# Kernel tuning notes

Measured on AMD Instinct MI355X. Metric: run time of the kernel, lower is better.

The kernel has to match this reference:

```python
import jax, jax.numpy as jnp
import numpy as np

DT = 0.1


def setup_inputs() -> dict:
    key = jax.random.key(0)
    k1, k2, k3, k4 = jax.random.split(key, 4)
    B, T, I, H, O = 32, 1024, 256, 512, 256
    return {
        "x": jax.random.normal(k1, (B, T, I), dtype=jnp.float32),
        "input_weights": jax.random.normal(k2, (H, I), dtype=jnp.float32) * (1.0 / np.sqrt(I)),
        "recurrent_weights": jax.random.normal(k3, (H, H), dtype=jnp.float32) * (1.0 / np.sqrt(H)),
        "time_constants": jnp.ones((H,), dtype=jnp.float32) + 0.1,
        "output_weights": jax.random.normal(k4, (O, H), dtype=jnp.float32) * (1.0 / np.sqrt(H)),
        "bias": jnp.zeros((H,), dtype=jnp.float32),
    }


def reference(x, input_weights, recurrent_weights, time_constants, output_weights, bias):
    B = x.shape[0]
    H = recurrent_weights.shape[0]
    h0 = jnp.zeros((B, H), dtype=x.dtype)

    # Precompute the input projection for all timesteps at once: (B,T,I)@(I,H) -> (T,B,H)
    sensory_all = jnp.einsum("bti,hi->tbh", x, input_weights)

    def step(hidden, sensory):
        # sensory: (B, H)
        recurrent = hidden @ recurrent_weights.T                      # (B, H)
        adaptive_tau = jax.nn.softplus(
            time_constants + 0.1 * jnp.mean(jnp.abs(sensory), axis=0)
        )                                                             # (H,)
        activation = jnp.tanh(sensory + recurrent + bias)             # (B, H)
        dhidden_dt = -hidden / adaptive_tau[None, :] + activation
        hidden = hidden + DT * dhidden_dt
        out_t = hidden @ output_weights.T                             # (B, O)
        return hidden, out_t

    final_hidden, outputs = jax.lax.scan(step, h0, sensory_all)        # outputs: (T, B, O)
    output = jnp.transpose(outputs, (1, 0, 2))                          # (B, T, O)
    return output, final_hidden
```

## Files before the change

### kernel.cpp

```cpp
#include <hip/hip_runtime.h>
#include <cstddef>

#define B_ 32
#define T_ 1024
#define IN_ 256
#define H_ 512
#define O_ 256
#define DT_ 0.1f

typedef _Float16 half2_t __attribute__((ext_vector_type(2)));

__device__ __forceinline__ float fdot2(half2_t a, half2_t b, float c) {
#if defined(__has_builtin)
#if __has_builtin(__builtin_amdgcn_fdot2)
    return __builtin_amdgcn_fdot2(a, b, c, false);
#else
    return c + (float)a[0] * (float)b[0] + (float)a[1] * (float)b[1];
#endif
#else
    return c + (float)a[0] * (float)b[0] + (float)a[1] * (float)b[1];
#endif
}

__device__ __forceinline__ half2_t cvt2(float x, float y) {
    half2_t r; r[0] = (_Float16)x; r[1] = (_Float16)y; return r;
}

__device__ __forceinline__ half2_t as_h2(float f) {
    union { float f; half2_t h; } u; u.f = f; return u.h;
}

template<int N, int K, bool SWA, bool SWC>
__global__ __launch_bounds__(256, 4) void gemm128(const float* __restrict__ A,
                                                  const float* __restrict__ Bw,
                                                  float* __restrict__ C) {
    __shared__ float al[32][132];
    __shared__ float bl[32][132];
    const int tid = threadIdx.x;
    const int m0 = blockIdx.x * 128;
    const int n0 = blockIdx.y * 128;
    const int tx = tid & 15;
    const int ty = tid >> 4;
    float acc[8][8] = {};

    const int lrow = tid >> 3;
    const int kk = (tid & 7) * 4;

    for (int kc = 0; kc < K; kc += 32) {
        __syncthreads();
#pragma unroll
        for (int p = 0; p < 4; ++p) {
            const int row = lrow + p * 32;
            const int m = m0 + row;
            const size_t aoff = SWA ? ((size_t)((m & 31) * T_ + (m >> 5)) * K)
                                    : ((size_t)m * K);
            const float4 v = *(const float4*)(A + aoff + kc + kk);
            al[kk + 0][row] = v.x; al[kk + 1][row] = v.y;
            al[kk + 2][row] = v.z; al[kk + 3][row] = v.w;
        }
#pragma unroll
        for (int p = 0; p < 4; ++p) {
            const int row = lrow + p * 32;
            const float4 v = *(const float4*)(Bw + (size_t)(n0 + row) * K + kc + kk);
            bl[kk + 0][row] = v.x; bl[kk + 1][row] = v.y;
            bl[kk + 2][row] = v.z; bl[kk + 3][row] = v.w;
        }
        __syncthreads();
#pragma unroll
        for (int k = 0; k < 32; ++k) {
            float av[8], bv[8];
            *(float4*)&av[0] = *(const float4*)&al[k][ty * 8];
            *(float4*)&av[4] = *(const float4*)&al[k][ty * 8 + 4];
            *(float4*)&bv[0] = *(const float4*)&bl[k][tx * 8];
            *(float4*)&bv[4] = *(const float4*)&bl[k][tx * 8 + 4];
#pragma unroll
            for (int i = 0; i < 8; ++i)
#pragma unroll
                for (int j = 0; j < 8; ++j)
                    acc[i][j] = fmaf(av[i], bv[j], acc[i][j]);
        }
    }
#pragma unroll
    for (int i = 0; i < 8; ++i) {
        const int m = m0 + ty * 8 + i;
        const size_t coff = SWC ? ((size_t)((m & 31) * T_ + (m >> 5)) * N)
                                : ((size_t)m * N);
        const float4 v0 = make_float4(acc[i][0], acc[i][1], acc[i][2], acc[i][3]);
        const float4 v1 = make_float4(acc[i][4], acc[i][5], acc[i][6], acc[i][7]);
        *(float4*)(C + coff + n0 + tx * 8) = v0;
        *(float4*)(C + coff + n0 + tx * 8 + 4) = v1;
    }
}

__global__ __launch_bounds__(512) void tau_kernel(const float* __restrict__ sens,
                                                  const float* __restrict__ tc,
                                                  float* __restrict__ acoef) {
    const int t = blockIdx.x;
    const int h = threadIdx.x;
    float s = 0.f;
#pragma unroll 8
    for (int b = 0; b < B_; ++b)
        s += fabsf(sens[((size_t)t * B_ + b) * H_ + h]);
    const float x = tc[h] + 0.1f * (s * (1.f / 32.f));
    const float sp = fmaxf(x, 0.f) + log1pf(expf(-fabsf(x)));
    acoef[(size_t)t * H_ + h] = 1.f - DT_ / sp;
}

#define RG_ 12
#define LG_ 4
#define SMEM_W   131072
#define SMEM_P   8192
#define SMEM_H   1024
#define SMEM_TOT (SMEM_W + SMEM_P + SMEM_H)

__global__ __launch_bounds__(512, 2) void scan_kernel(
    const float* __restrict__ Wr, const float* __restrict__ acoef,
    const float* __restrict__ bias, float* sensH, float* __restrict__ finalh) {
    extern __shared__ char smem[];
    half2_t* wlds = (half2_t*)smem;
    float* pred   = (float*)(smem + SMEM_W);
    _Float16* h2s = (_Float16*)(smem + SMEM_W + SMEM_P);

    const int tid = threadIdx.x;
    const int b = blockIdx.x;
    const int w = tid >> 6;
    const int c = w >> 1;
    const int rg = ((w & 1) << 6) | (tid & 63);
    const int row0 = rg * 4;
    const int col0 = c * 128;

    half2_t wr[4][RG_ * 4];
#pragma unroll
    for (int r = 0; r < 4; ++r) {
        const float* wrow = Wr + (size_t)(row0 + r) * H_ + col0;
#pragma unroll
        for (int d = 0; d < RG_ * 4; ++d) {
            const float2 v = *(const float2*)(wrow + 2 * d);
            wr[r][d] = cvt2(v.x, v.y);
        }
#pragma unroll
        for (int g = 0; g < LG_; ++g) {
#pragma unroll
            for (int j = 0; j < 4; ++j) {
                const float2 v = *(const float2*)(wrow + 2 * ((RG_ + g) * 4 + j));
                wlds[((size_t)(g * 4 + r) * 512 + tid) * 4 + j] = cvt2(v.x, v.y);
            }
        }
    }

    if (tid < 256) ((half2_t*)h2s)[tid] = cvt2(0.f, 0.f);
    float h_reg = 0.f;
    const float bias_r = bias[tid];
    float s_cur = sensH[(size_t)b * H_ + tid];
    float a_cur = acoef[tid];
    __syncthreads();

    const half2_t* h2c = (const half2_t*)h2s + c * 64;

    for (int t = 0; t < T_; ++t) {
        const int tn = (t < T_ - 1) ? t + 1 : t;
        const float s_nxt = sensH[((size_t)tn * B_ + b) * H_ + tid];
        const float a_nxt = acoef[(size_t)tn * H_ + tid];

        float acc[4] = {0.f, 0.f, 0.f, 0.f};
#pragma unroll
        for (int g = 0; g < RG_; ++g) {
            const float4 hv = *(const float4*)(h2c + g * 4);
            const half2_t hh[4] = {as_h2(hv.x), as_h2(hv.y), as_h2(hv.z), as_h2(hv.w)};
#pragma unroll
            for (int r = 0; r < 4; ++r)
#pragma unroll
                for (int j = 0; j < 4; ++j)
                    acc[r] = fdot2(wr[r][g * 4 + j], hh[j], acc[r]);
        }
#pragma unroll
        for (int g = 0; g < LG_; ++g) {
            const float4 hv = *(const float4*)(h2c + (RG_ + g) * 4);
            const half2_t hh[4] = {as_h2(hv.x), as_h2(hv.y), as_h2(hv.z), as_h2(hv.w)};
#pragma unroll
            for (int r = 0; r < 4; ++r) {
                const float4 wv = *(const float4*)(wlds + ((size_t)(g * 4 + r) * 512 + tid) * 4);
                acc[r] = fdot2(as_h2(wv.x), hh[0], acc[r]);
                acc[r] = fdot2(as_h2(wv.y), hh[1], acc[r]);
                acc[r] = fdot2(as_h2(wv.z), hh[2], acc[r]);
                acc[r] = fdot2(as_h2(wv.w), hh[3], acc[r]);
            }
        }
        *(float4*)(pred + c * 512 + row0) = make_float4(acc[0], acc[1], acc[2], acc[3]);
        __syncthreads();

        const float rec = pred[tid] + pred[512 + tid] + pred[1024 + tid] + pred[1536 + tid];
        const float act = tanhf(s_cur + rec + bias_r);
        h_reg = a_cur * h_reg + DT_ * act;
        sensH[((size_t)t * B_ + b) * H_ + tid] = h_reg;
        h2s[tid] = (_Float16)h_reg;
        s_cur = s_nxt;
        a_cur = a_nxt;
        __syncthreads();
    }
    finalh[(size_t)b * H_ + tid] = h_reg;
}

extern "C" void kernel_launch(void* const* d_in, const int* in_sizes, int n_in,
                              void* d_out, int out_size, void* d_ws, size_t ws_size,
                              hipStream_t stream) {
    const float* x    = (const float*)d_in[0];
    const float* Win  = (const float*)d_in[1];
    const float* Wr   = (const float*)d_in[2];
    const float* tc   = (const float*)d_in[3];
    const float* Wo   = (const float*)d_in[4];
    const float* bias = (const float*)d_in[5];
    float* out = (float*)d_out;

    float* sensH = (float*)d_ws;
    float* acoef = sensH + (size_t)T_ * B_ * H_;
    const size_t need = ((size_t)T_ * B_ * H_ + (size_t)T_ * H_) * sizeof(float);
    if (ws_size < need) return;

    (void)hipFuncSetAttribute((const void*)scan_kernel,
                              hipFuncAttributeMaxDynamicSharedMemorySize, SMEM_TOT);

    {
        dim3 grid(32768 / 128, H_ / 128);
        hipLaunchKernelGGL((gemm128<H_, IN_, true, false>), grid, dim3(256), 0, stream,
                           x, Win, sensH);
    }
    hipLaunchKernelGGL(tau_kernel, dim3(T_), dim3(H_), 0, stream, sensH, tc, acoef);
    hipLaunchKernelGGL(scan_kernel, dim3(B_), dim3(512), SMEM_TOT, stream,
                       Wr, acoef, bias, sensH, out + (size_t)B_ * T_ * O_);
    {
        dim3 grid(32768 / 128, O_ / 128);
        hipLaunchKernelGGL((gemm128<O_, H_, false, true>), grid, dim3(256), 0, stream,
                           sensH, Wo, out);
    }
}
```

Before: 1.837 ms.

## Double scan block to 1024 threads, halving per-thread recurrent column slice

The recurrent scan kernel now runs 1024 threads per batch element instead of 512, with 8 column groups of 64 instead of 4 of 128. Each thread holds half as many fp16 weight pairs in registers and reads a smaller LDS slice, which shortens each thread's serial dot-product chain per timestep. In exchange, the cross-group reduction in the pred buffer doubles to 8 partial sums, block-wide barriers now span 16 waves, and only half the threads do the elementwise update. Register pressure under the larger block size is also a risk.

Result: slower. 2.412 ms (+31.3%).

```diff
diff --git a/kernel.cpp b/kernel.cpp
--- a/kernel.cpp
+++ b/kernel.cpp
@@ -106,14 +106,13 @@
     acoef[(size_t)t * H_ + h] = 1.f - DT_ / sp;
 }
 
-#define RG_ 12
-#define LG_ 4
+#define RGC_ 24
 #define SMEM_W   131072
-#define SMEM_P   8192
+#define SMEM_P   16384
 #define SMEM_H   1024
 #define SMEM_TOT (SMEM_W + SMEM_P + SMEM_H)
 
-__global__ __launch_bounds__(512, 2) void scan_kernel(
+__global__ __launch_bounds__(1024, 4) void scan_kernel(
     const float* __restrict__ Wr, const float* __restrict__ acoef,
     const float* __restrict__ bias, float* sensH, float* __restrict__ finalh) {
     extern __shared__ char smem[];
@@ -127,44 +126,50 @@
     const int c = w >> 1;
     const int rg = ((w & 1) << 6) | (tid & 63);
     const int row0 = rg * 4;
-    const int col0 = c * 128;
-
-    half2_t wr[4][RG_ * 4];
+    const int col0 = c * 64;
+
+    half2_t wr[4][RGC_];
 #pragma unroll
     for (int r = 0; r < 4; ++r) {
         const float* wrow = Wr + (size_t)(row0 + r) * H_ + col0;
 #pragma unroll
-        for (int d = 0; d < RG_ * 4; ++d) {
+        for (int d = 0; d < RGC_; ++d) {
             const float2 v = *(const float2*)(wrow + 2 * d);
             wr[r][d] = cvt2(v.x, v.y);
         }
 #pragma unroll
-        for (int g = 0; g < LG_; ++g) {
+        for (int g = 0; g < 2; ++g) {
 #pragma unroll
             for (int j = 0; j < 4; ++j) {
-                const float2 v = *(const float2*)(wrow + 2 * ((RG_ + g) * 4 + j));
-                wlds[((size_t)(g * 4 + r) * 512 + tid) * 4 + j] = cvt2(v.x, v.y);
+                const float2 v = *(const float2*)(wrow + 48 + 8 * g + 2 * j);
+                wlds[((size_t)(g * 4 + r) * 1024 + tid) * 4 + j] = cvt2(v.x, v.y);
             }
         }
     }
 
-    if (tid < 256) ((half2_t*)h2s)[tid] = cvt2(0.f, 0.f);
-    float h_reg = 0.f;
-    const float bias_r = bias[tid];
-    float s_cur = sensH[(size_t)b * H_ + tid];
-    float a_cur = acoef[tid];
+    float h_reg = 0.f, s_cur = 0.f, a_cur = 0.f, bias_r = 0.f;
+    if (tid < H_) {
+        ((half2_t*)h2s)[tid & 255] = cvt2(0.f, 0.f);
+        if (tid < 256) ((half2_t*)h2s)[tid] = cvt2(0.f, 0.f);
+        bias_r = bias[tid];
+        s_cur = sensH[(size_t)b * H_ + tid];
+        a_cur = acoef[tid];
+    }
     __syncthreads();
 
-    const half2_t* h2c = (const half2_t*)h2s + c * 64;
+    const half2_t* h2c = (const half2_t*)h2s + c * 32;
 
     for (int t = 0; t < T_; ++t) {
-        const int tn = (t < T_ - 1) ? t + 1 : t;
-        const float s_nxt = sensH[((size_t)tn * B_ + b) * H_ + tid];
-        const float a_nxt = acoef[(size_t)tn * H_ + tid];
+        float s_nxt = 0.f, a_nxt = 0.f;
+        if (tid < H_) {
+            const int tn = (t < T_ - 1) ? t + 1 : t;
+            s_nxt = sensH[((size_t)tn * B_ + b) * H_ + tid];
+            a_nxt = acoef[(size_t)tn * H_ + tid];
+        }
 
         float acc[4] = {0.f, 0.f, 0.f, 0.f};
 #pragma unroll
-        for (int g = 0; g < RG_; ++g) {
+        for (int g = 0; g < 6; ++g) {
             const float4 hv = *(const float4*)(h2c + g * 4);
             const half2_t hh[4] = {as_h2(hv.x), as_h2(hv.y), as_h2(hv.z), as_h2(hv.w)};
 #pragma unroll
@@ -174,12 +179,12 @@
                     acc[r] = fdot2(wr[r][g * 4 + j], hh[j], acc[r]);
         }
 #pragma unroll
-        for (int g = 0; g < LG_; ++g) {
-            const float4 hv = *(const float4*)(h2c + (RG_ + g) * 4);
+        for (int g = 0; g < 2; ++g) {
+            const float4 hv = *(const float4*)(h2c + 24 + g * 4);
             const half2_t hh[4] = {as_h2(hv.x), as_h2(hv.y), as_h2(hv.z), as_h2(hv.w)};
 #pragma unroll
             for (int r = 0; r < 4; ++r) {
-                const float4 wv = *(const float4*)(wlds + ((size_t)(g * 4 + r) * 512 + tid) * 4);
+                const float4 wv = *(const float4*)(wlds + ((size_t)(g * 4 + r) * 1024 + tid) * 4);
                 acc[r] = fdot2(as_h2(wv.x), hh[0], acc[r]);
                 acc[r] = fdot2(as_h2(wv.y), hh[1], acc[r]);
                 acc[r] = fdot2(as_h2(wv.z), hh[2], acc[r]);
@@ -189,16 +194,20 @@
         *(float4*)(pred + c * 512 + row0) = make_float4(acc[0], acc[1], acc[2], acc[3]);
         __syncthreads();
 
-        const float rec = pred[tid] + pred[512 + tid] + pred[1024 + tid] + pred[1536 + tid];
-        const float act = tanhf(s_cur + rec + bias_r);
-        h_reg = a_cur * h_reg + DT_ * act;
-        sensH[((size_t)t * B_ + b) * H_ + tid] = h_reg;
-        h2s[tid] = (_Float16)h_reg;
-        s_cur = s_nxt;
-        a_cur = a_nxt;
-        __syncthreads();
-    }
-    finalh[(size_t)b * H_ + tid] = h_reg;
+        if (tid < H_) {
+            float rec = 0.f;
+#pragma unroll
+            for (int cc = 0; cc < 8; ++cc) rec += pred[cc * 512 + tid];
+            const float act = tanhf(s_cur + rec + bias_r);
+            h_reg = a_cur * h_reg + DT_ * act;
+            sensH[((size_t)t * B_ + b) * H_ + tid] = h_reg;
+            h2s[tid] = (_Float16)h_reg;
+            s_cur = s_nxt;
+            a_cur = a_nxt;
+        }
+        __syncthreads();
+    }
+    if (tid < H_) finalh[(size_t)b * H_ + tid] = h_reg;
 }
 
 extern "C" void kernel_launch(void* const* d_in, const int* in_sizes, int n_in,
@@ -226,7 +235,7 @@
                            x, Win, sensH);
     }
     hipLaunchKernelGGL(tau_kernel, dim3(T_), dim3(H_), 0, stream, sensH, tc, acoef);
-    hipLaunchKernelGGL(scan_kernel, dim3(B_), dim3(512), SMEM_TOT, stream,
+    hipLaunchKernelGGL(scan_kernel, dim3(B_), dim3(1024), SMEM_TOT, stream,
                        Wr, acoef, bias, sensH, out + (size_t)B_ * T_ * O_);
     {
         dim3 grid(32768 / 128, O_ / 128);
```

## Broadcast hidden state via scalar loads from global instead of LDS

Applied to the files above, without the earlier changes.

Writes the fp16 hidden state to a global scratch buffer (borrowed from the output area) and reads it each step with scalar dwordx16 loads after invalidating the scalar cache. The dot products then take the hidden values as SGPR operands in inline-asm v_dot2, removing the per-step LDS reads of h. This trades LDS bandwidth for L2 round-trip latency on a serial dependency chain. It also risks visibility issues between vector stores and scalar loads across the barrier.

Measured after the change: 1.891 ms. +3.0%, slower.

```diff
diff --git a/kernel.cpp b/kernel.cpp
--- a/kernel.cpp
+++ b/kernel.cpp
@@ -1,5 +1,6 @@
 #include <hip/hip_runtime.h>
 #include <cstddef>
+#include <cstdint>
 
 #define B_ 32
 #define T_ 1024
@@ -9,23 +10,11 @@
 #define DT_ 0.1f
 
 typedef _Float16 half2_t __attribute__((ext_vector_type(2)));
-
-__device__ __forceinline__ float fdot2(half2_t a, half2_t b, float c) {
-#if defined(__has_builtin)
-#if __has_builtin(__builtin_amdgcn_fdot2)
-    return __builtin_amdgcn_fdot2(a, b, c, false);
-#else
-    return c + (float)a[0] * (float)b[0] + (float)a[1] * (float)b[1];
-#endif
-#else
-    return c + (float)a[0] * (float)b[0] + (float)a[1] * (float)b[1];
-#endif
-}
+typedef int v16i __attribute__((ext_vector_type(16)));
 
 __device__ __forceinline__ half2_t cvt2(float x, float y) {
     half2_t r; r[0] = (_Float16)x; r[1] = (_Float16)y; return r;
 }
-
 __device__ __forceinline__ half2_t as_h2(float f) {
     union { float f; half2_t h; } u; u.f = f; return u.h;
 }
@@ -106,96 +95,122 @@
     acoef[(size_t)t * H_ + h] = 1.f - DT_ / sp;
 }
 
-#define RG_ 12
-#define LG_ 4
-#define SMEM_W   131072
-#define SMEM_P   8192
-#define SMEM_H   1024
-#define SMEM_TOT (SMEM_W + SMEM_P + SMEM_H)
-
-__global__ __launch_bounds__(512, 2) void scan_kernel(
-    const float* __restrict__ Wr, const float* __restrict__ acoef,
-    const float* __restrict__ bias, float* sensH, float* __restrict__ finalh) {
+#define LDSW_BYTES (16 * 512 * 16)
+#define SMEM_TOT   (LDSW_BYTES + 4 * 512 * 4)
+
+#define DOT2SV(acc, hs, wv) \
+    asm("v_dot2_f32_f16 %0, %1, %2, %0" : "+v"(acc) : "s"(hs), "v"(wv))
+
+#define HV(k) ((k) < 16 ? h0[(k)] : (k) < 32 ? h1[(k) - 16] : \
+               (k) < 48 ? h2[(k) - 32] : h3[(k) - 48])
+
+__global__ __attribute__((amdgpu_flat_work_group_size(512, 512),
+                          amdgpu_waves_per_eu(2, 2)))
+void scan_kernel(const float* __restrict__ Wr, const float* __restrict__ acoef,
+                 const float* __restrict__ bias, float* sensH,
+                 float* __restrict__ finalh, _Float16* __restrict__ h2g) {
     extern __shared__ char smem[];
-    half2_t* wlds = (half2_t*)smem;
-    float* pred   = (float*)(smem + SMEM_W);
-    _Float16* h2s = (_Float16*)(smem + SMEM_W + SMEM_P);
-
-    const int tid = threadIdx.x;
-    const int b = blockIdx.x;
-    const int w = tid >> 6;
-    const int c = w >> 1;
-    const int rg = ((w & 1) << 6) | (tid & 63);
-    const int row0 = rg * 4;
-    const int col0 = c * 128;
-
-    half2_t wr[4][RG_ * 4];
+    half2_t* wl = (half2_t*)smem;
+    float* pred = (float*)(smem + LDSW_BYTES);
+
+    const int tid  = threadIdx.x;
+    const int b    = blockIdx.x;
+    const int lane = tid & 63;
+    const int w    = tid >> 6;
+    const int cw   = w & 3;
+    const int rh   = w >> 2;
+    const int row0 = rh * 256 + lane * 4;
+    const int col0 = cw * 128;
+
+    half2_t wr[4][48];
 #pragma unroll
     for (int r = 0; r < 4; ++r) {
         const float* wrow = Wr + (size_t)(row0 + r) * H_ + col0;
 #pragma unroll
-        for (int d = 0; d < RG_ * 4; ++d) {
-            const float2 v = *(const float2*)(wrow + 2 * d);
-            wr[r][d] = cvt2(v.x, v.y);
-        }
-#pragma unroll
-        for (int g = 0; g < LG_; ++g) {
+        for (int k = 0; k < 48; ++k) {
+            const float2 v = *(const float2*)(wrow + 2 * k);
+            wr[r][k] = cvt2(v.x, v.y);
+        }
+#pragma unroll
+        for (int pp = 0; pp < 4; ++pp)
 #pragma unroll
             for (int j = 0; j < 4; ++j) {
-                const float2 v = *(const float2*)(wrow + 2 * ((RG_ + g) * 4 + j));
-                wlds[((size_t)(g * 4 + r) * 512 + tid) * 4 + j] = cvt2(v.x, v.y);
+                const int k = 48 + pp * 4 + j;
+                const float2 v = *(const float2*)(wrow + 2 * k);
+                wl[((size_t)(r * 4 + pp) * 512 + tid) * 4 + j] = cvt2(v.x, v.y);
             }
-        }
-    }
-
-    if (tid < 256) ((half2_t*)h2s)[tid] = cvt2(0.f, 0.f);
+    }
+
+    if (tid < 256) ((half2_t*)(h2g + (size_t)b * H_))[tid] = cvt2(0.f, 0.f);
+
     float h_reg = 0.f;
     const float bias_r = bias[tid];
     float s_cur = sensH[(size_t)b * H_ + tid];
     float a_cur = acoef[tid];
+
+    const uint64_t hp_u = (uint64_t)(uintptr_t)(h2g + (size_t)b * H_ + col0);
+    const uint32_t hp_lo = __builtin_amdgcn_readfirstlane((uint32_t)hp_u);
+    const uint32_t hp_hi = __builtin_amdgcn_readfirstlane((uint32_t)(hp_u >> 32));
+    const uint64_t hp_s = ((uint64_t)hp_hi << 32) | hp_lo;
+
     __syncthreads();
-
-    const half2_t* h2c = (const half2_t*)h2s + c * 64;
 
     for (int t = 0; t < T_; ++t) {
         const int tn = (t < T_ - 1) ? t + 1 : t;
         const float s_nxt = sensH[((size_t)tn * B_ + b) * H_ + tid];
         const float a_nxt = acoef[(size_t)tn * H_ + tid];
 
+        v16i h0, h1, h2, h3;
+        asm volatile(
+            "s_dcache_inv\n\t"
+            "s_load_dwordx16 %0, %4, 0x0\n\t"
+            "s_load_dwordx16 %1, %4, 0x40\n\t"
+            "s_load_dwordx16 %2, %4, 0x80\n\t"
+            "s_load_dwordx16 %3, %4, 0xc0\n\t"
+            "s_waitcnt lgkmcnt(0)"
+            : "=s"(h0), "=s"(h1), "=s"(h2), "=s"(h3)
+            : "s"(hp_s));
+
         float acc[4] = {0.f, 0.f, 0.f, 0.f};
 #pragma unroll
-        for (int g = 0; g < RG_; ++g) {
-            const float4 hv = *(const float4*)(h2c + g * 4);
-            const half2_t hh[4] = {as_h2(hv.x), as_h2(hv.y), as_h2(hv.z), as_h2(hv.w)};
-#pragma unroll
-            for (int r = 0; r < 4; ++r)
-#pragma unroll
-                for (int j = 0; j < 4; ++j)
-                    acc[r] = fdot2(wr[r][g * 4 + j], hh[j], acc[r]);
-        }
-#pragma unroll
-        for (int g = 0; g < LG_; ++g) {
-            const float4 hv = *(const float4*)(h2c + (RG_ + g) * 4);
-            const half2_t hh[4] = {as_h2(hv.x), as_h2(hv.y), as_h2(hv.z), as_h2(hv.w)};
-#pragma unroll
-            for (int r = 0; r < 4; ++r) {
-                const float4 wv = *(const float4*)(wlds + ((size_t)(g * 4 + r) * 512 + tid) * 4);
-                acc[r] = fdot2(as_h2(wv.x), hh[0], acc[r]);
-                acc[r] = fdot2(as_h2(wv.y), hh[1], acc[r]);
-                acc[r] = fdot2(as_h2(wv.z), hh[2], acc[r]);
-                acc[r] = fdot2(as_h2(wv.w), hh[3], acc[r]);
-            }
-        }
-        *(float4*)(pred + c * 512 + row0) = make_float4(acc[0], acc[1], acc[2], acc[3]);
-        __syncthreads();
-
-        const float rec = pred[tid] + pred[512 + tid] + pred[1024 + tid] + pred[1536 + tid];
-        const float act = tanhf(s_cur + rec + bias_r);
-        h_reg = a_cur * h_reg + DT_ * act;
-        sensH[((size_t)t * B_ + b) * H_ + tid] = h_reg;
-        h2s[tid] = (_Float16)h_reg;
-        s_cur = s_nxt;
-        a_cur = a_nxt;
+        for (int r = 0; r < 4; ++r) {
+            const float4 wv0 = *(const float4*)(wl + ((size_t)(r * 4 + 0) * 512 + tid) * 4);
+            const float4 wv1 = *(const float4*)(wl + ((size_t)(r * 4 + 1) * 512 + tid) * 4);
+            const float4 wv2 = *(const float4*)(wl + ((size_t)(r * 4 + 2) * 512 + tid) * 4);
+            const float4 wv3 = *(const float4*)(wl + ((size_t)(r * 4 + 3) * 512 + tid) * 4);
+#pragma unroll
+            for (int k = 0; k < 48; ++k) DOT2SV(acc[r], HV(k), wr[r][k]);
+            DOT2SV(acc[r], HV(48), as_h2(wv0.x));
+            DOT2SV(acc[r], HV(49), as_h2(wv0.y));
+            DOT2SV(acc[r], HV(50), as_h2(wv0.z));
+            DOT2SV(acc[r], HV(51), as_h2(wv0.w));
+            DOT2SV(acc[r], HV(52), as_h2(wv1.x));
+            DOT2SV(acc[r], HV(53), as_h2(wv1.y));
+            DOT2SV(acc[r], HV(54), as_h2(wv1.z));
+            DOT2SV(acc[r], HV(55), as_h2(wv1.w));
+            DOT2SV(acc[r], HV(56), as_h2(wv2.x));
+            DOT2SV(acc[r], HV(57), as_h2(wv2.y));
+            DOT2SV(acc[r], HV(58), as_h2(wv2.z));
+            DOT2SV(acc[r], HV(59), as_h2(wv2.w));
+            DOT2SV(acc[r], HV(60), as_h2(wv3.x));
+            DOT2SV(acc[r], HV(61), as_h2(wv3.y));
+            DOT2SV(acc[r], HV(62), as_h2(wv3.z));
+            DOT2SV(acc[r], HV(63), as_h2(wv3.w));
+        }
+        *(float4*)(pred + cw * 512 + row0) =
+            make_float4(acc[0], acc[1], acc[2], acc[3]);
+        __syncthreads();
+
+        {
+            const float rec = pred[tid] + pred[512 + tid] +
+                              pred[1024 + tid] + pred[1536 + tid];
+            const float act = tanhf(s_cur + rec + bias_r);
+            h_reg = a_cur * h_reg + DT_ * act;
+            sensH[((size_t)t * B_ + b) * H_ + tid] = h_reg;
+            h2g[(size_t)b * H_ + tid] = (_Float16)h_reg;
+            s_cur = s_nxt;
+            a_cur = a_nxt;
+        }
         __syncthreads();
     }
     finalh[(size_t)b * H_ + tid] = h_reg;
@@ -217,6 +232,8 @@
     const size_t need = ((size_t)T_ * B_ * H_ + (size_t)T_ * H_) * sizeof(float);
     if (ws_size < need) return;
 
+    _Float16* h2g = (_Float16*)d_out;
+
     (void)hipFuncSetAttribute((const void*)scan_kernel,
                               hipFuncAttributeMaxDynamicSharedMemorySize, SMEM_TOT);
 
@@ -227,7 +244,7 @@
     }
     hipLaunchKernelGGL(tau_kernel, dim3(T_), dim3(H_), 0, stream, sensH, tc, acoef);
     hipLaunchKernelGGL(scan_kernel, dim3(B_), dim3(512), SMEM_TOT, stream,
-                       Wr, acoef, bias, sensH, out + (size_t)B_ * T_ * O_);
+                       Wr, acoef, bias, sensH, out + (size_t)B_ * T_ * O_, h2g);
     {
         dim3 grid(32768 / 128, O_ / 128);
         hipLaunchKernelGGL((gemm128<O_, H_, false, true>), grid, dim3(256), 0, stream,
```
